# Optimization experiments

Measured on AMD Instinct MI355X. Metric: run time of the kernel, lower is better.

Reference implementation:

```python
import jax, jax.numpy as jnp
import numpy as np

B, NX, NLQ = 2, 2048, 64
D_IN, D_OUT, H = 768, 768, 12
HD = D_OUT // H  # 64
P_X, P_LQ = 0.1, 0.2  # dropout probs for x-x block vs any learnable-query block
DROP_KEY = 42  # fixed key for dropout masks (training mode)


def setup_inputs() -> dict:
    key = jax.random.key(0)
    ks = jax.random.split(key, 6)
    s = 0.02
    return {
        "x": jax.random.normal(ks[0], (B, NX, D_IN), jnp.float32),
        "learnable_queries": jax.random.normal(ks[1], (B, NLQ, D_IN), jnp.float32),
        "Wq": jax.random.normal(ks[2], (D_IN, D_OUT), jnp.float32) * s,
        "Wk": jax.random.normal(ks[3], (D_IN, D_OUT), jnp.float32) * s,
        "Wv": jax.random.normal(ks[4], (D_IN, D_OUT), jnp.float32) * s,
        "Wo": jax.random.normal(ks[5], (D_OUT, D_OUT), jnp.float32) * s,
        "bo": jnp.zeros((D_OUT,), jnp.float32),
    }


def reference(x, learnable_queries, Wq, Wk, Wv, Wo, bo):
    b, nx, _ = x.shape
    nlq = learnable_queries.shape[1]
    T = nx + nlq
    inp = jnp.concatenate([x, learnable_queries], axis=1)  # [b, T, d_in]

    def to_heads(W):
        return (inp @ W).reshape(b, T, H, HD).transpose(0, 2, 1, 3)  # [b, H, T, hd]

    q, k, v = to_heads(Wq), to_heads(Wk), to_heads(Wv)

    scores = jnp.einsum('bhqd,bhkd->bhqk', q, k) / np.float32(np.sqrt(HD))
    w = jax.nn.softmax(scores, axis=-1)  # [b, H, T, T]

    # --- block-structured dropout (training mode) ---
    kp_x = 1.0 - P_X
    kp_lq = 1.0 - P_LQ
    is_x = jnp.arange(T) < nx
    # keep prob is kp_x on the x-x block, kp_lq on the three lq-involving blocks
    keep_p = jnp.where(is_x[:, None] & is_x[None, :], kp_x, kp_lq)  # [T, T]
    u = jax.random.uniform(jax.random.key(DROP_KEY), (b, H, T, T), jnp.float32)
    mask = (u < keep_p).astype(w.dtype)
    n_xx = nx * nx
    n_lq_total = T * T - n_xx
    scale = (T * T) / (n_xx * kp_x + n_lq_total * kp_lq)
    w = w * mask * jnp.asarray(scale, w.dtype)

    ctx = jnp.einsum('bhqk,bhkd->bhqd', w, v)           # [b, H, T, hd]
    ctx = ctx.transpose(0, 2, 1, 3).reshape(b, T, D_OUT)  # [b, T, d_out]
    return ctx @ Wo + bo
```

## Files before the change

kernel.cpp:

```cpp
#include <hip/hip_runtime.h>
#include <stdint.h>

#define B_ 2
#define NX_ 2048
#define NLQ_ 64
#define T_ 2112
#define DIN_ 768
#define DOUT_ 768
#define NH_ 12
#define HD_ 64

#define QSZ_ ((size_t)3244032)
#define HALF_U 53526528u
#define SCALE_ ((float)(4460544.0 / (4194304.0 * 0.9 + 266240.0 * 0.8)))
#define WPR_ 66
#define MWPB_ 1408u
#define K_X_ 7549747u
#define K_LQ_ 6710887u

typedef __attribute__((ext_vector_type(8))) short bf16x8;
typedef __attribute__((ext_vector_type(4))) float f32x4;
typedef unsigned int uint32;

__device__ __forceinline__ uint32 rotl_(uint32 x, uint32 r) {
  return (x << r) | (x >> (32u - r));
}

__device__ __forceinline__ uint2 threefry_(uint32 x0, uint32 x1) {
  const uint32 ks0 = 0u, ks1 = 42u;
  const uint32 ks2 = 0x1BD11BDAu ^ ks0 ^ ks1;
  x0 += ks0; x1 += ks1;
#define TFR_(r) { x0 += x1; x1 = rotl_(x1, (r)); x1 ^= x0; }
  TFR_(13) TFR_(15) TFR_(26) TFR_(6)
  x0 += ks1; x1 += ks2 + 1u;
  TFR_(17) TFR_(29) TFR_(16) TFR_(24)
  x0 += ks2; x1 += ks0 + 2u;
  TFR_(13) TFR_(15) TFR_(26) TFR_(6)
  x0 += ks0; x1 += ks1 + 3u;
  TFR_(17) TFR_(29) TFR_(16) TFR_(24)
  x0 += ks1; x1 += ks2 + 4u;
  TFR_(13) TFR_(15) TFR_(26) TFR_(6)
  x0 += ks2; x1 += ks0 + 5u;
#undef TFR_
  return make_uint2(x0, x1);
}

__device__ __forceinline__ unsigned short f2b_(float f) {
  const uint32 u = __float_as_uint(f);
  return (unsigned short)((u + 0x7FFFu + ((u >> 16) & 1u)) >> 16);
}
__device__ __forceinline__ uint32 pack2_(float lo, float hi) {
  return (uint32)f2b_(lo) | ((uint32)f2b_(hi) << 16);
}

__global__ __launch_bounds__(256) void prep_kernel(
    const float* __restrict__ Wq, const float* __restrict__ Wk,
    const float* __restrict__ Wv, const float* __restrict__ Wo,
    unsigned short* __restrict__ Wt) {
  __shared__ float Tf[64][65];
  const int tid = threadIdx.x;
  const int k0 = blockIdx.x << 6;
  const int n0 = blockIdx.y << 6;
  const int mat = blockIdx.z;
  const float* Wm = (mat == 0) ? Wq : (mat == 1) ? Wk : (mat == 2) ? Wv : Wo;
  const int r = tid >> 2;
  const int cch = (tid & 3) << 4;
  const float* src = Wm + (size_t)(k0 + r) * DOUT_ + n0 + cch;
#pragma unroll
  for (int j = 0; j < 4; ++j) {
    const float4 v = *(const float4*)(src + 4 * j);
    Tf[r][cch + 4 * j + 0] = v.x; Tf[r][cch + 4 * j + 1] = v.y;
    Tf[r][cch + 4 * j + 2] = v.z; Tf[r][cch + 4 * j + 3] = v.w;
  }
  __syncthreads();
  float f[16];
#pragma unroll
  for (int j = 0; j < 16; ++j) f[j] = Tf[cch + j][r];
  uint4 o0, o1;
  o0.x = pack2_(f[0], f[1]);  o0.y = pack2_(f[2], f[3]);
  o0.z = pack2_(f[4], f[5]);  o0.w = pack2_(f[6], f[7]);
  o1.x = pack2_(f[8], f[9]);  o1.y = pack2_(f[10], f[11]);
  o1.z = pack2_(f[12], f[13]); o1.w = pack2_(f[14], f[15]);
  unsigned short* dst = Wt + ((size_t)mat * DOUT_ + n0 + r) * DIN_ + k0 + cch;
  *(uint4*)dst = o0;
  *(uint4*)(dst + 8) = o1;
}

__global__ __launch_bounds__(256) void qkv_kernel(
    const float* __restrict__ xg, const float* __restrict__ lqg,
    const unsigned short* __restrict__ Wt,
    unsigned short* __restrict__ Qh, unsigned short* __restrict__ Kh,
    unsigned short* __restrict__ Vth, uint32* __restrict__ Mask) {
  __shared__ unsigned short AsB[4096];
  __shared__ unsigned short BsB[4096];
  const int tid = threadIdx.x;
  const int w = tid >> 6;
  const int lane = tid & 63;
  const int c = lane & 15;
  const int g = lane >> 4;
  const int m0 = blockIdx.x << 6;
  const int wsel = blockIdx.y / NH_;
  const int h = blockIdx.y % NH_;

  const int ar = tid >> 2;
  const int kpart = (tid & 3) << 4;
  const float* arow;
  {
    const int m = m0 + ar;
    const int bb = m / T_;
    const int tt = m - bb * T_;
    arow = (tt < NX_) ? (xg + ((size_t)bb * NX_ + tt) * DIN_)
                      : (lqg + ((size_t)bb * NLQ_ + (tt - NX_)) * DIN_);
  }
  const unsigned short* brow = Wt + ((size_t)wsel * DOUT_ + h * HD_ + ar) * DIN_;
  const int wrA = ar * 128;
  const int swzS = (ar & 7) << 4;
  const int swzF = (c & 7) << 4;

  f32x4 ac0 = {0.f, 0.f, 0.f, 0.f}, ac1 = ac0, ac2 = ac0, ac3 = ac0;

  for (int k0 = 0; k0 < DIN_; k0 += 64) {
    const float4 a0 = *(const float4*)(arow + k0 + kpart);
    const float4 a1 = *(const float4*)(arow + k0 + kpart + 4);
    const float4 a2 = *(const float4*)(arow + k0 + kpart + 8);
    const float4 a3 = *(const float4*)(arow + k0 + kpart + 12);
    const uint4 b01 = *(const uint4*)(brow + k0 + kpart);
    const uint4 b23 = *(const uint4*)(brow + k0 + kpart + 8);
    uint4 pa0, pa1;
    pa0.x = pack2_(a0.x, a0.y); pa0.y = pack2_(a0.z, a0.w);
    pa0.z = pack2_(a1.x, a1.y); pa0.w = pack2_(a1.z, a1.w);
    pa1.x = pack2_(a2.x, a2.y); pa1.y = pack2_(a2.z, a2.w);
    pa1.z = pack2_(a3.x, a3.y); pa1.w = pack2_(a3.z, a3.w);
    __syncthreads();
    *(uint4*)((char*)AsB + wrA + ((kpart * 2) ^ swzS)) = pa0;
    *(uint4*)((char*)AsB + wrA + ((kpart * 2 + 16) ^ swzS)) = pa1;
    *(uint4*)((char*)BsB + wrA + ((kpart * 2) ^ swzS)) = b01;
    *(uint4*)((char*)BsB + wrA + ((kpart * 2 + 16) ^ swzS)) = b23;
    __syncthreads();
#pragma unroll
    for (int s = 0; s < 2; ++s) {
      const int off = ((s << 6) | (g << 4)) ^ swzF;
      const bf16x8 af = *(const bf16x8*)((const char*)AsB + (16 * w + c) * 128 + off);
      const bf16x8 b0 = *(const bf16x8*)((const char*)BsB + (c) * 128 + off);
      const bf16x8 b1 = *(const bf16x8*)((const char*)BsB + (c + 16) * 128 + off);
      const bf16x8 b2 = *(const bf16x8*)((const char*)BsB + (c + 32) * 128 + off);
      const bf16x8 b3 = *(const bf16x8*)((const char*)BsB + (c + 48) * 128 + off);
      ac0 = __builtin_amdgcn_mfma_f32_16x16x32_bf16(af, b0, ac0, 0, 0, 0);
      ac1 = __builtin_amdgcn_mfma_f32_16x16x32_bf16(af, b1, ac1, 0, 0, 0);
      ac2 = __builtin_amdgcn_mfma_f32_16x16x32_bf16(af, b2, ac2, 0, 0, 0);
      ac3 = __builtin_amdgcn_mfma_f32_16x16x32_bf16(af, b3, ac3, 0, 0, 0);
    }
  }

  const int bb2 = m0 / T_;
  const int tb = m0 - bb2 * T_;
  const size_t rowBase = (size_t)(bb2 * NH_ + h) * T_;
  if (wsel == 0) {
#pragma unroll
    for (int i = 0; i < 4; ++i) {
      const size_t rr = (rowBase + tb + 16 * w + 4 * g + i) * HD_ + c;
      Qh[rr +  0] = f2b_(ac0[i] * 0.125f);
      Qh[rr + 16] = f2b_(ac1[i] * 0.125f);
      Qh[rr + 32] = f2b_(ac2[i] * 0.125f);
      Qh[rr + 48] = f2b_(ac3[i] * 0.125f);
    }
  } else if (wsel == 1) {
#pragma unroll
    for (int i = 0; i < 4; ++i) {
      const size_t rr = (rowBase + tb + 16 * w + 4 * g + i) * HD_ + c;
      Kh[rr +  0] = f2b_(ac0[i]);
      Kh[rr + 16] = f2b_(ac1[i]);
      Kh[rr + 32] = f2b_(ac2[i]);
      Kh[rr + 48] = f2b_(ac3[i]);
    }
  } else {
    __syncthreads();
#pragma unroll
    for (int i = 0; i < 4; ++i) {
      const int col2 = (16 * w + 4 * g + i) * 2;
      *(unsigned short*)((char*)AsB + (c)      * 128 + (col2 ^ ((c & 7) << 4))) = f2b_(ac0[i]);
      *(unsigned short*)((char*)AsB + (c + 16) * 128 + (col2 ^ ((c & 7) << 4))) = f2b_(ac1[i]);
      *(unsigned short*)((char*)AsB + (c + 32) * 128 + (col2 ^ ((c & 7) << 4))) = f2b_(ac2[i]);
      *(unsigned short*)((char*)AsB + (c + 48) * 128 + (col2 ^ ((c & 7) << 4))) = f2b_(ac3[i]);
    }
    __syncthreads();
    const int hd = tid >> 2;
    const int tch = (tid & 3) << 4;
    const uint4 v0 = *(const uint4*)((const char*)AsB + hd * 128 + ((tch * 2) ^ ((hd & 7) << 4)));
    const uint4 v1 = *(const uint4*)((const char*)AsB + hd * 128 + ((tch * 2 + 16) ^ ((hd & 7) << 4)));
    unsigned short* dst = Vth + ((size_t)(bb2 * NH_ + h) * HD_ + hd) * T_ + tb + tch;
    *(uint4*)dst = v0;
    *(uint4*)(dst + 8) = v1;
  }

  const uint32 wbeg = (uint32)(blockIdx.y * 66 + blockIdx.x) * MWPB_;
  for (uint32 wI = wbeg + (uint32)tid; wI < wbeg + MWPB_; wI += 256u) {
    const uint32 rowIdx = wI / WPR_;
    const uint32 jw = wI - rowIdx * WPR_;
    const uint32 bI = rowIdx / (NH_ * T_);
    const uint32 rem = rowIdx - bI * (NH_ * T_);
    const uint32 iQ = rem % T_;
    const uint32 c0 = bI * HALF_U + rem * (uint32)T_ + jw * 32u;
    const uint32 thr = ((iQ < NX_) && (jw < 64u)) ? K_X_ : K_LQ_;
    uint32 word = 0u;
#pragma unroll 4
    for (int k = 0; k < 32; ++k) {
      const uint2 y = threefry_(0u, c0 + (uint32)k);
      word |= (((y.x ^ y.y) >> 9) < thr ? 1u : 0u) << k;
    }
    Mask[wI] = word;
  }
}

__global__ __launch_bounds__(128) void attn_kernel(
    const unsigned short* __restrict__ Qh, const unsigned short* __restrict__ Kh,
    const unsigned short* __restrict__ Vth, const uint32* __restrict__ Mask,
    float* __restrict__ ctx) {
  __shared__ unsigned short KsU[4096];
  __shared__ unsigned short VsU[4096];
  __shared__ unsigned short PsU[2 * 1152];
  const int tid = threadIdx.x;
  const int w = tid >> 6;
  const int lane = tid & 63;
  const int c = lane & 15;
  const int g = lane >> 4;
  const int q0 = blockIdx.x << 5;
  const int h = blockIdx.y;
  const int b = blockIdx.z;
  const size_t hbT = (size_t)(b * NH_ + h) * T_;
  const size_t vbase = (size_t)(b * NH_ + h) * HD_;

  bf16x8 aq0, aq1;
  {
    const unsigned short* qrow = Qh + (hbT + q0 + 16 * w + c) * HD_ + (g << 3);
    aq0 = *(const bf16x8*)(qrow);
    aq1 = *(const bf16x8*)(qrow + 32);
  }
  f32x4 ca0 = {0.f, 0.f, 0.f, 0.f}, ca1 = ca0, ca2 = ca0, ca3 = ca0;
  float lacc[4] = {0.f, 0.f, 0.f, 0.f};
  uint32 wb[4];
#pragma unroll
  for (int i = 0; i < 4; ++i)
    wb[i] = ((uint32)b * HALF_U +
             (uint32)(h * T_ + q0 + 16 * w + 4 * g + i) * (uint32)T_) >> 5;

  const int psE = w * 1152;
  const int psB = w * 2304;
  const int swz = (c & 7) << 4;

  for (int kt = 0; kt < T_; kt += 64) {
#pragma unroll
    for (int ii = 0; ii < 4; ++ii) {
      const int seg = tid + (ii << 7);
      const int srow = seg >> 3;
      const int sc = (seg & 7) << 3;
      const uint4 kv4 = *(const uint4*)(Kh + (hbT + kt + srow) * HD_ + sc);
      *(uint4*)((char*)KsU + srow * 128 + ((sc * 2) ^ ((srow & 7) << 4))) = kv4;
      const uint4 vv4 = *(const uint4*)(Vth + (vbase + srow) * T_ + kt + sc);
      *(uint4*)((char*)VsU + srow * 128 + ((sc * 2) ^ ((srow & 7) << 4))) = vv4;
    }
    __syncthreads();

    f32x4 sa0 = {0.f, 0.f, 0.f, 0.f}, sa1 = sa0, sa2 = sa0, sa3 = sa0;
#pragma unroll
    for (int s = 0; s < 2; ++s) {
      const int off = ((s << 6) | (g << 4)) ^ swz;
      const bf16x8 bk0 = *(const bf16x8*)((const char*)KsU + (c) * 128 + off);
      const bf16x8 bk1 = *(const bf16x8*)((const char*)KsU + (c + 16) * 128 + off);
      const bf16x8 bk2 = *(const bf16x8*)((const char*)KsU + (c + 32) * 128 + off);
      const bf16x8 bk3 = *(const bf16x8*)((const char*)KsU + (c + 48) * 128 + off);
      const bf16x8 aqs = s ? aq1 : aq0;
      sa0 = __builtin_amdgcn_mfma_f32_16x16x32_bf16(aqs, bk0, sa0, 0, 0, 0);
      sa1 = __builtin_amdgcn_mfma_f32_16x16x32_bf16(aqs, bk1, sa1, 0, 0, 0);
      sa2 = __builtin_amdgcn_mfma_f32_16x16x32_bf16(aqs, bk2, sa2, 0, 0, 0);
      sa3 = __builtin_amdgcn_mfma_f32_16x16x32_bf16(aqs, bk3, sa3, 0, 0, 0);
    }

    const uint32 ktw = (uint32)(kt >> 5);
#pragma unroll
    for (int n = 0; n < 4; ++n) {
      const f32x4 sv = (n == 0) ? sa0 : (n == 1) ? sa1 : (n == 2) ? sa2 : sa3;
      const int sh = ((n & 1) << 4) + c;
      const uint32 wOff = ktw + (n >> 1);
#pragma unroll
      for (int i = 0; i < 4; ++i) {
        const float pe = __expf(sv[i]);
        lacc[i] += pe;
        const uint32 word = Mask[wb[i] + wOff];
        PsU[psE + (4 * g + i) * 72 + 16 * n + c] =
            ((word >> sh) & 1u) ? f2b_(pe) : (unsigned short)0;
      }
    }
    __syncthreads();

    const bf16x8 ap0 = *(const bf16x8*)((const char*)PsU + psB + c * 144 + (g << 4));
    const bf16x8 ap1 = *(const bf16x8*)((const char*)PsU + psB + c * 144 + 64 + (g << 4));
#pragma unroll
    for (int s = 0; s < 2; ++s) {
      const int off = ((s << 6) | (g << 4)) ^ swz;
      const bf16x8 bv0 = *(const bf16x8*)((const char*)VsU + (c) * 128 + off);
      const bf16x8 bv1 = *(const bf16x8*)((const char*)VsU + (c + 16) * 128 + off);
      const bf16x8 bv2 = *(const bf16x8*)((const char*)VsU + (c + 32) * 128 + off);
      const bf16x8 bv3 = *(const bf16x8*)((const char*)VsU + (c + 48) * 128 + off);
      const bf16x8 aps = s ? ap1 : ap0;
      ca0 = __builtin_amdgcn_mfma_f32_16x16x32_bf16(aps, bv0, ca0, 0, 0, 0);
      ca1 = __builtin_amdgcn_mfma_f32_16x16x32_bf16(aps, bv1, ca1, 0, 0, 0);
      ca2 = __builtin_amdgcn_mfma_f32_16x16x32_bf16(aps, bv2, ca2, 0, 0, 0);
      ca3 = __builtin_amdgcn_mfma_f32_16x16x32_bf16(aps, bv3, ca3, 0, 0, 0);
    }
    __syncthreads();
  }

#pragma unroll
  for (int i = 0; i < 4; ++i) {
    float li = lacc[i];
    li += __shfl_xor(li, 1);
    li += __shfl_xor(li, 2);
    li += __shfl_xor(li, 4);
    li += __shfl_xor(li, 8);
    const float inv = SCALE_ / li;
    float* dst = ctx + (size_t)(b * T_ + q0 + 16 * w + 4 * g + i) * DOUT_ + (h << 6) + c;
    dst[0]  = ca0[i] * inv;
    dst[16] = ca1[i] * inv;
    dst[32] = ca2[i] * inv;
    dst[48] = ca3[i] * inv;
  }
}

__global__ __launch_bounds__(256) void oproj_kernel(
    const float* __restrict__ ctxm, const unsigned short* __restrict__ Wt,
    const float* __restrict__ bo, float* __restrict__ out) {
  __shared__ unsigned short AsB[4096];
  __shared__ unsigned short BsB[4096];
  const int tid = threadIdx.x;
  const int w = tid >> 6;
  const int lane = tid & 63;
  const int c = lane & 15;
  const int g = lane >> 4;
  const int m0 = blockIdx.x << 6;
  const int n0 = blockIdx.y << 6;
  const int ar = tid >> 2;
  const int kpart = (tid & 3) << 4;
  const float* arow = ctxm + (size_t)(m0 + ar) * DIN_;
  const unsigned short* brow = Wt + ((size_t)3 * DOUT_ + n0 + ar) * DIN_;
  const int wrA = ar * 128;
  const int swzS = (ar & 7) << 4;
  const int swzF = (c & 7) << 4;

  f32x4 ac0 = {0.f, 0.f, 0.f, 0.f}, ac1 = ac0, ac2 = ac0, ac3 = ac0;
  for (int k0 = 0; k0 < DIN_; k0 += 64) {
    const float4 a0 = *(const float4*)(arow + k0 + kpart);
    const float4 a1 = *(const float4*)(arow + k0 + kpart + 4);
    const float4 a2 = *(const float4*)(arow + k0 + kpart + 8);
    const float4 a3 = *(const float4*)(arow + k0 + kpart + 12);
    const uint4 b01 = *(const uint4*)(brow + k0 + kpart);
    const uint4 b23 = *(const uint4*)(brow + k0 + kpart + 8);
    uint4 pa0, pa1;
    pa0.x = pack2_(a0.x, a0.y); pa0.y = pack2_(a0.z, a0.w);
    pa0.z = pack2_(a1.x, a1.y); pa0.w = pack2_(a1.z, a1.w);
    pa1.x = pack2_(a2.x, a2.y); pa1.y = pack2_(a2.z, a2.w);
    pa1.z = pack2_(a3.x, a3.y); pa1.w = pack2_(a3.z, a3.w);
    __syncthreads();
    *(uint4*)((char*)AsB + wrA + ((kpart * 2) ^ swzS)) = pa0;
    *(uint4*)((char*)AsB + wrA + ((kpart * 2 + 16) ^ swzS)) = pa1;
    *(uint4*)((char*)BsB + wrA + ((kpart * 2) ^ swzS)) = b01;
    *(uint4*)((char*)BsB + wrA + ((kpart * 2 + 16) ^ swzS)) = b23;
    __syncthreads();
#pragma unroll
    for (int s = 0; s < 2; ++s) {
      const int off = ((s << 6) | (g << 4)) ^ swzF;
      const bf16x8 af = *(const bf16x8*)((const char*)AsB + (16 * w + c) * 128 + off);
      const bf16x8 b0 = *(const bf16x8*)((const char*)BsB + (c) * 128 + off);
      const bf16x8 b1 = *(const bf16x8*)((const char*)BsB + (c + 16) * 128 + off);
      const bf16x8 b2 = *(const bf16x8*)((const char*)BsB + (c + 32) * 128 + off);
      const bf16x8 b3 = *(const bf16x8*)((const char*)BsB + (c + 48) * 128 + off);
      ac0 = __builtin_amdgcn_mfma_f32_16x16x32_bf16(af, b0, ac0, 0, 0, 0);
      ac1 = __builtin_amdgcn_mfma_f32_16x16x32_bf16(af, b1, ac1, 0, 0, 0);
      ac2 = __builtin_amdgcn_mfma_f32_16x16x32_bf16(af, b2, ac2, 0, 0, 0);
      ac3 = __builtin_amdgcn_mfma_f32_16x16x32_bf16(af, b3, ac3, 0, 0, 0);
    }
  }
  const float bi0 = bo[n0 + c];
  const float bi1 = bo[n0 + 16 + c];
  const float bi2 = bo[n0 + 32 + c];
  const float bi3 = bo[n0 + 48 + c];
#pragma unroll
  for (int i = 0; i < 4; ++i) {
    float* dst = out + (size_t)(m0 + 16 * w + 4 * g + i) * DOUT_ + n0 + c;
    dst[0]  = ac0[i] + bi0;
    dst[16] = ac1[i] + bi1;
    dst[32] = ac2[i] + bi2;
    dst[48] = ac3[i] + bi3;
  }
}

extern "C" void kernel_launch(void* const* d_in, const int* in_sizes, int n_in,
                              void* d_out, int out_size, void* d_ws, size_t ws_size,
                              hipStream_t stream) {
  (void)in_sizes; (void)n_in; (void)out_size; (void)ws_size;
  const float* x  = (const float*)d_in[0];
  const float* lq = (const float*)d_in[1];
  const float* Wq = (const float*)d_in[2];
  const float* Wk = (const float*)d_in[3];
  const float* Wv = (const float*)d_in[4];
  const float* Wo = (const float*)d_in[5];
  const float* bo = (const float*)d_in[6];
  unsigned short* Qh  = (unsigned short*)d_ws;
  unsigned short* Kh  = Qh + QSZ_;
  unsigned short* Vth = Kh + QSZ_;
  float* Cb = (float*)(Vth + QSZ_);
  unsigned short* Wt = (unsigned short*)(Cb + QSZ_);
  uint32* Mask = (uint32*)((char*)d_ws + 37158912);
  prep_kernel<<<dim3(12, 12, 4), dim3(256), 0, stream>>>(Wq, Wk, Wv, Wo, Wt);
  qkv_kernel<<<dim3(66, 36), dim3(256), 0, stream>>>(x, lq, Wt, Qh, Kh, Vth, Mask);
  attn_kernel<<<dim3(66, NH_, B_), dim3(128), 0, stream>>>(Qh, Kh, Vth, Mask, Cb);
  oproj_kernel<<<dim3(66, 12), dim3(256), 0, stream>>>(Cb, Wt, bo, (float*)d_out);
}
```

Measured before the change: 472.3 us.

## Pre-convert inputs to bf16, fuse QKV per head, ballot-based mask, wider attention blocks

A new kernel converts x and the learnable queries to bf16 once, so the QKV GEMM no longer repeats the fp32-to-bf16 packing for each of the 36 weight column blocks. The QKV kernel now computes Q, K and V for one head in a single block, reusing the A tile across 12 MFMA column tiles. The dropout mask generation changes from a per-thread loop over 32 bits to one threefry call per lane with wave ballots, thresholding full 32-bit values. The attention kernel doubles to 64 queries and 4 waves per block, halving K/V tile reloads at the cost of fewer blocks and more registers and LDS per block.

```diff
diff --git a/kernel.cpp b/kernel.cpp
--- a/kernel.cpp
+++ b/kernel.cpp
@@ -13,10 +13,8 @@
 #define QSZ_ ((size_t)3244032)
 #define HALF_U 53526528u
 #define SCALE_ ((float)(4460544.0 / (4194304.0 * 0.9 + 266240.0 * 0.8)))
-#define WPR_ 66
-#define MWPB_ 1408u
-#define K_X_ 7549747u
-#define K_LQ_ 6710887u
+#define KXS_ 3865470464u
+#define KLQS_ 3435974144u
 
 typedef __attribute__((ext_vector_type(8))) short bf16x8;
 typedef __attribute__((ext_vector_type(4))) float f32x4;
@@ -53,6 +51,24 @@
   return (uint32)f2b_(lo) | ((uint32)f2b_(hi) << 16);
 }
 
+__global__ __launch_bounds__(256) void xconv_kernel(
+    const float* __restrict__ xg, const float* __restrict__ lqg,
+    unsigned short* __restrict__ Xb) {
+  const uint32 f = (blockIdx.x * 256u + threadIdx.x) * 8u;
+  const uint32 m = f / 768u;
+  const uint32 col = f - m * 768u;
+  const uint32 bb = (m >= (uint32)T_) ? 1u : 0u;
+  const uint32 tt = m - bb * (uint32)T_;
+  const float* src = (tt < NX_) ? (xg + ((size_t)bb * NX_ + tt) * DIN_ + col)
+                                : (lqg + ((size_t)bb * NLQ_ + (tt - NX_)) * DIN_ + col);
+  const float4 a = *(const float4*)(src);
+  const float4 b = *(const float4*)(src + 4);
+  uint4 o;
+  o.x = pack2_(a.x, a.y); o.y = pack2_(a.z, a.w);
+  o.z = pack2_(b.x, b.y); o.w = pack2_(b.z, b.w);
+  *(uint4*)(Xb + f) = o;
+}
+
 __global__ __launch_bounds__(256) void prep_kernel(
     const float* __restrict__ Wq, const float* __restrict__ Wk,
     const float* __restrict__ Wv, const float* __restrict__ Wo,
@@ -87,144 +103,139 @@
 }
 
 __global__ __launch_bounds__(256) void qkv_kernel(
-    const float* __restrict__ xg, const float* __restrict__ lqg,
-    const unsigned short* __restrict__ Wt,
+    const unsigned short* __restrict__ Xb, const unsigned short* __restrict__ Wt,
     unsigned short* __restrict__ Qh, unsigned short* __restrict__ Kh,
     unsigned short* __restrict__ Vth, uint32* __restrict__ Mask) {
   __shared__ unsigned short AsB[4096];
-  __shared__ unsigned short BsB[4096];
+  __shared__ unsigned short BsB[12288];
   const int tid = threadIdx.x;
   const int w = tid >> 6;
   const int lane = tid & 63;
   const int c = lane & 15;
   const int g = lane >> 4;
   const int m0 = blockIdx.x << 6;
-  const int wsel = blockIdx.y / NH_;
-  const int h = blockIdx.y % NH_;
-
-  const int ar = tid >> 2;
-  const int kpart = (tid & 3) << 4;
-  const float* arow;
-  {
-    const int m = m0 + ar;
-    const int bb = m / T_;
-    const int tt = m - bb * T_;
-    arow = (tt < NX_) ? (xg + ((size_t)bb * NX_ + tt) * DIN_)
-                      : (lqg + ((size_t)bb * NLQ_ + (tt - NX_)) * DIN_);
-  }
-  const unsigned short* brow = Wt + ((size_t)wsel * DOUT_ + h * HD_ + ar) * DIN_;
-  const int wrA = ar * 128;
-  const int swzS = (ar & 7) << 4;
+  const int h  = blockIdx.y;
+
+  const int srow = tid >> 2;
+  const int seg  = (tid & 3) << 5;
+  const int swzR = ((srow & 7) << 4);
   const int swzF = (c & 7) << 4;
 
-  f32x4 ac0 = {0.f, 0.f, 0.f, 0.f}, ac1 = ac0, ac2 = ac0, ac3 = ac0;
+  f32x4 acc[12];
+#pragma unroll
+  for (int nt = 0; nt < 12; ++nt) acc[nt] = (f32x4){0.f, 0.f, 0.f, 0.f};
+
+  const unsigned short* arow = Xb + (size_t)(m0 + srow) * DIN_;
 
   for (int k0 = 0; k0 < DIN_; k0 += 64) {
-    const float4 a0 = *(const float4*)(arow + k0 + kpart);
-    const float4 a1 = *(const float4*)(arow + k0 + kpart + 4);
-    const float4 a2 = *(const float4*)(arow + k0 + kpart + 8);
-    const float4 a3 = *(const float4*)(arow + k0 + kpart + 12);
-    const uint4 b01 = *(const uint4*)(brow + k0 + kpart);
-    const uint4 b23 = *(const uint4*)(brow + k0 + kpart + 8);
-    uint4 pa0, pa1;
-    pa0.x = pack2_(a0.x, a0.y); pa0.y = pack2_(a0.z, a0.w);
-    pa0.z = pack2_(a1.x, a1.y); pa0.w = pack2_(a1.z, a1.w);
-    pa1.x = pack2_(a2.x, a2.y); pa1.y = pack2_(a2.z, a2.w);
-    pa1.z = pack2_(a3.x, a3.y); pa1.w = pack2_(a3.z, a3.w);
-    __syncthreads();
-    *(uint4*)((char*)AsB + wrA + ((kpart * 2) ^ swzS)) = pa0;
-    *(uint4*)((char*)AsB + wrA + ((kpart * 2 + 16) ^ swzS)) = pa1;
-    *(uint4*)((char*)BsB + wrA + ((kpart * 2) ^ swzS)) = b01;
-    *(uint4*)((char*)BsB + wrA + ((kpart * 2 + 16) ^ swzS)) = b23;
+    const uint4 a0 = *(const uint4*)(arow + k0 + (seg >> 1));
+    const uint4 a1 = *(const uint4*)(arow + k0 + (seg >> 1) + 8);
+    uint4 b0[3], b1[3];
+#pragma unroll
+    for (int ii = 0; ii < 3; ++ii) {
+      const int n = srow + (ii << 6);
+      const unsigned short* brow =
+          Wt + ((size_t)(n >> 6) * DOUT_ + h * HD_ + (n & 63)) * DIN_ + k0 + (seg >> 1);
+      b0[ii] = *(const uint4*)(brow);
+      b1[ii] = *(const uint4*)(brow + 8);
+    }
+    __syncthreads();
+    *(uint4*)((char*)AsB + srow * 128 + (seg ^ swzR)) = a0;
+    *(uint4*)((char*)AsB + srow * 128 + ((seg + 16) ^ swzR)) = a1;
+#pragma unroll
+    for (int ii = 0; ii < 3; ++ii) {
+      const int n = srow + (ii << 6);
+      *(uint4*)((char*)BsB + n * 128 + (seg ^ swzR)) = b0[ii];
+      *(uint4*)((char*)BsB + n * 128 + ((seg + 16) ^ swzR)) = b1[ii];
+    }
     __syncthreads();
 #pragma unroll
     for (int s = 0; s < 2; ++s) {
       const int off = ((s << 6) | (g << 4)) ^ swzF;
       const bf16x8 af = *(const bf16x8*)((const char*)AsB + (16 * w + c) * 128 + off);
-      const bf16x8 b0 = *(const bf16x8*)((const char*)BsB + (c) * 128 + off);
-      const bf16x8 b1 = *(const bf16x8*)((const char*)BsB + (c + 16) * 128 + off);
-      const bf16x8 b2 = *(const bf16x8*)((const char*)BsB + (c + 32) * 128 + off);
-      const bf16x8 b3 = *(const bf16x8*)((const char*)BsB + (c + 48) * 128 + off);
-      ac0 = __builtin_amdgcn_mfma_f32_16x16x32_bf16(af, b0, ac0, 0, 0, 0);
-      ac1 = __builtin_amdgcn_mfma_f32_16x16x32_bf16(af, b1, ac1, 0, 0, 0);
-      ac2 = __builtin_amdgcn_mfma_f32_16x16x32_bf16(af, b2, ac2, 0, 0, 0);
-      ac3 = __builtin_amdgcn_mfma_f32_16x16x32_bf16(af, b3, ac3, 0, 0, 0);
-    }
+#pragma unroll
+      for (int nt = 0; nt < 12; ++nt) {
+        const bf16x8 bf = *(const bf16x8*)((const char*)BsB + (nt * 16 + c) * 128 + off);
+        acc[nt] = __builtin_amdgcn_mfma_f32_16x16x32_bf16(af, bf, acc[nt], 0, 0, 0);
+      }
+    }
+    __syncthreads();
   }
 
   const int bb2 = m0 / T_;
   const int tb = m0 - bb2 * T_;
-  const size_t rowBase = (size_t)(bb2 * NH_ + h) * T_;
-  if (wsel == 0) {
-#pragma unroll
-    for (int i = 0; i < 4; ++i) {
-      const size_t rr = (rowBase + tb + 16 * w + 4 * g + i) * HD_ + c;
-      Qh[rr +  0] = f2b_(ac0[i] * 0.125f);
-      Qh[rr + 16] = f2b_(ac1[i] * 0.125f);
-      Qh[rr + 32] = f2b_(ac2[i] * 0.125f);
-      Qh[rr + 48] = f2b_(ac3[i] * 0.125f);
-    }
-  } else if (wsel == 1) {
-#pragma unroll
-    for (int i = 0; i < 4; ++i) {
-      const size_t rr = (rowBase + tb + 16 * w + 4 * g + i) * HD_ + c;
-      Kh[rr +  0] = f2b_(ac0[i]);
-      Kh[rr + 16] = f2b_(ac1[i]);
-      Kh[rr + 32] = f2b_(ac2[i]);
-      Kh[rr + 48] = f2b_(ac3[i]);
-    }
-  } else {
-    __syncthreads();
+  const size_t rowBase = (size_t)(bb2 * NH_ + h) * T_ + tb;
+#pragma unroll
+  for (int nt = 0; nt < 4; ++nt)
+#pragma unroll
+    for (int i = 0; i < 4; ++i)
+      Qh[(rowBase + 16 * w + 4 * g + i) * HD_ + nt * 16 + c] = f2b_(acc[nt][i] * 0.125f);
+#pragma unroll
+  for (int nt = 4; nt < 8; ++nt)
+#pragma unroll
+    for (int i = 0; i < 4; ++i)
+      Kh[(rowBase + 16 * w + 4 * g + i) * HD_ + (nt - 4) * 16 + c] = f2b_(acc[nt][i]);
+#pragma unroll
+  for (int nt = 8; nt < 12; ++nt) {
+    const int hd = (nt - 8) * 16 + c;
 #pragma unroll
     for (int i = 0; i < 4; ++i) {
       const int col2 = (16 * w + 4 * g + i) * 2;
-      *(unsigned short*)((char*)AsB + (c)      * 128 + (col2 ^ ((c & 7) << 4))) = f2b_(ac0[i]);
-      *(unsigned short*)((char*)AsB + (c + 16) * 128 + (col2 ^ ((c & 7) << 4))) = f2b_(ac1[i]);
-      *(unsigned short*)((char*)AsB + (c + 32) * 128 + (col2 ^ ((c & 7) << 4))) = f2b_(ac2[i]);
-      *(unsigned short*)((char*)AsB + (c + 48) * 128 + (col2 ^ ((c & 7) << 4))) = f2b_(ac3[i]);
-    }
-    __syncthreads();
+      *(unsigned short*)((char*)AsB + hd * 128 + (col2 ^ swzF)) = f2b_(acc[nt][i]);
+    }
+  }
+  __syncthreads();
+  {
     const int hd = tid >> 2;
-    const int tch = (tid & 3) << 4;
-    const uint4 v0 = *(const uint4*)((const char*)AsB + hd * 128 + ((tch * 2) ^ ((hd & 7) << 4)));
-    const uint4 v1 = *(const uint4*)((const char*)AsB + hd * 128 + ((tch * 2 + 16) ^ ((hd & 7) << 4)));
-    unsigned short* dst = Vth + ((size_t)(bb2 * NH_ + h) * HD_ + hd) * T_ + tb + tch;
+    const int ch = (tid & 3) << 5;
+    const uint4 v0 = *(const uint4*)((const char*)AsB + hd * 128 + (ch ^ ((hd & 7) << 4)));
+    const uint4 v1 = *(const uint4*)((const char*)AsB + hd * 128 + ((ch + 16) ^ ((hd & 7) << 4)));
+    unsigned short* dst = Vth + ((size_t)(bb2 * NH_ + h) * HD_ + hd) * T_ + tb + (ch >> 1);
     *(uint4*)dst = v0;
     *(uint4*)(dst + 8) = v1;
   }
 
-  const uint32 wbeg = (uint32)(blockIdx.y * 66 + blockIdx.x) * MWPB_;
-  for (uint32 wI = wbeg + (uint32)tid; wI < wbeg + MWPB_; wI += 256u) {
-    const uint32 rowIdx = wI / WPR_;
-    const uint32 jw = wI - rowIdx * WPR_;
-    const uint32 bI = rowIdx / (NH_ * T_);
-    const uint32 rem = rowIdx - bI * (NH_ * T_);
-    const uint32 iQ = rem % T_;
-    const uint32 c0 = bI * HALF_U + rem * (uint32)T_ + jw * 32u;
-    const uint32 thr = ((iQ < NX_) && (jw < 64u)) ? K_X_ : K_LQ_;
-    uint32 word = 0u;
-#pragma unroll 4
-    for (int k = 0; k < 32; ++k) {
-      const uint2 y = threefry_(0u, c0 + (uint32)k);
-      word |= (((y.x ^ y.y) >> 9) < thr ? 1u : 0u) << k;
-    }
-    Mask[wI] = word;
-  }
-}
-
-__global__ __launch_bounds__(128) void attn_kernel(
+  const uint32 wvbeg = (uint32)(blockIdx.y * 66 + blockIdx.x) * 4224u + (uint32)w * 1056u;
+  for (uint32 wI = wvbeg; wI < wvbeg + 1056u; wI += 4u) {
+    const uint32 b0 = wI * 32u;
+    const uint32 g0 = b0 + (uint32)lane;
+    const uint32 g1 = g0 + 64u;
+    uint32 thrS0, thrS1;
+    {
+      const uint32 row0 = b0 / 2112u;
+      const uint32 cb0 = b0 - row0 * 2112u;
+      thrS0 = ((row0 % 2112u) < 2048u && cb0 < 2048u) ? KXS_ : KLQS_;
+      const uint32 b1 = b0 + 64u;
+      const uint32 row1 = b1 / 2112u;
+      const uint32 cb1 = b1 - row1 * 2112u;
+      thrS1 = ((row1 % 2112u) < 2048u && cb1 < 2048u) ? KXS_ : KLQS_;
+    }
+    const uint2 ya = threefry_(0u, g0);
+    const uint2 yb = threefry_(0u, g1);
+    const unsigned long long balA = __ballot((ya.x ^ ya.y) < thrS0);
+    const unsigned long long balB = __ballot((yb.x ^ yb.y) < thrS1);
+    if (lane == 0) {
+      uint4 st;
+      st.x = (uint32)balA; st.y = (uint32)(balA >> 32);
+      st.z = (uint32)balB; st.w = (uint32)(balB >> 32);
+      *(uint4*)(Mask + wI) = st;
+    }
+  }
+}
+
+__global__ __launch_bounds__(256) void attn_kernel(
     const unsigned short* __restrict__ Qh, const unsigned short* __restrict__ Kh,
     const unsigned short* __restrict__ Vth, const uint32* __restrict__ Mask,
     float* __restrict__ ctx) {
   __shared__ unsigned short KsU[4096];
   __shared__ unsigned short VsU[4096];
-  __shared__ unsigned short PsU[2 * 1152];
+  __shared__ unsigned short PsU[4 * 1152];
   const int tid = threadIdx.x;
   const int w = tid >> 6;
   const int lane = tid & 63;
   const int c = lane & 15;
   const int g = lane >> 4;
-  const int q0 = blockIdx.x << 5;
+  const int q0 = blockIdx.x << 6;
   const int h = blockIdx.y;
   const int b = blockIdx.z;
   const size_t hbT = (size_t)(b * NH_ + h) * T_;
@@ -250,8 +261,8 @@
 
   for (int kt = 0; kt < T_; kt += 64) {
 #pragma unroll
-    for (int ii = 0; ii < 4; ++ii) {
-      const int seg = tid + (ii << 7);
+    for (int ii = 0; ii < 2; ++ii) {
+      const int seg = tid + (ii << 8);
       const int srow = seg >> 3;
       const int sc = (seg & 7) << 3;
       const uint4 kv4 = *(const uint4*)(Kh + (hbT + kt + srow) * HD_ + sc);
@@ -409,10 +420,12 @@
   unsigned short* Kh  = Qh + QSZ_;
   unsigned short* Vth = Kh + QSZ_;
   float* Cb = (float*)(Vth + QSZ_);
+  unsigned short* Xb = (unsigned short*)Cb;
   unsigned short* Wt = (unsigned short*)(Cb + QSZ_);
   uint32* Mask = (uint32*)((char*)d_ws + 37158912);
+  xconv_kernel<<<dim3(1584), dim3(256), 0, stream>>>(x, lq, Xb);
   prep_kernel<<<dim3(12, 12, 4), dim3(256), 0, stream>>>(Wq, Wk, Wv, Wo, Wt);
-  qkv_kernel<<<dim3(66, 36), dim3(256), 0, stream>>>(x, lq, Wt, Qh, Kh, Vth, Mask);
-  attn_kernel<<<dim3(66, NH_, B_), dim3(128), 0, stream>>>(Qh, Kh, Vth, Mask, Cb);
+  qkv_kernel<<<dim3(66, 12), dim3(256), 0, stream>>>(Xb, Wt, Qh, Kh, Vth, Mask);
+  attn_kernel<<<dim3(33, NH_, B_), dim3(256), 0, stream>>>(Qh, Kh, Vth, Mask, Cb);
   oproj_kernel<<<dim3(66, 12), dim3(256), 0, stream>>>(Cb, Wt, bo, (float*)d_out);
 }
```

New measurement: 598.2 us. +26.6%, slower.

## Pre-convert inputs to bf16, ballot-based dropout mask, larger attention tiles

Applied to the files above, without the earlier changes.

Adds a kernel that converts x and the learnable queries to bf16 once, so the QKV GEMM no longer repacks fp32 on every N-tile. It also swaps the QKV grid order so blocks sharing an input row tile run close together. The dropout mask generation now has each lane produce one threefry bit, combines bits with a wave ballot, and compares full 32-bit values against scaled thresholds. Attention now uses 64-query blocks with 256 threads and writes the context as bf16, which halves the context traffic into the output projection at some precision cost.

```diff
diff --git a/kernel.cpp b/kernel.cpp
--- a/kernel.cpp
+++ b/kernel.cpp
@@ -13,10 +13,8 @@
 #define QSZ_ ((size_t)3244032)
 #define HALF_U 53526528u
 #define SCALE_ ((float)(4460544.0 / (4194304.0 * 0.9 + 266240.0 * 0.8)))
-#define WPR_ 66
-#define MWPB_ 1408u
-#define K_X_ 7549747u
-#define K_LQ_ 6710887u
+#define KXS_ 3865470464u
+#define KLQS_ 3435974144u
 
 typedef __attribute__((ext_vector_type(8))) short bf16x8;
 typedef __attribute__((ext_vector_type(4))) float f32x4;
@@ -53,6 +51,24 @@
   return (uint32)f2b_(lo) | ((uint32)f2b_(hi) << 16);
 }
 
+__global__ __launch_bounds__(256) void xconv_kernel(
+    const float* __restrict__ xg, const float* __restrict__ lqg,
+    unsigned short* __restrict__ Xb) {
+  const uint32 f = (blockIdx.x * 256u + threadIdx.x) * 8u;
+  const uint32 m = f / 768u;
+  const uint32 col = f - m * 768u;
+  const uint32 bb = (m >= (uint32)T_) ? 1u : 0u;
+  const uint32 tt = m - bb * (uint32)T_;
+  const float* src = (tt < NX_) ? (xg + ((size_t)bb * NX_ + tt) * DIN_ + col)
+                                : (lqg + ((size_t)bb * NLQ_ + (tt - NX_)) * DIN_ + col);
+  const float4 a = *(const float4*)(src);
+  const float4 b = *(const float4*)(src + 4);
+  uint4 o;
+  o.x = pack2_(a.x, a.y); o.y = pack2_(a.z, a.w);
+  o.z = pack2_(b.x, b.y); o.w = pack2_(b.z, b.w);
+  *(uint4*)(Xb + f) = o;
+}
+
 __global__ __launch_bounds__(256) void prep_kernel(
     const float* __restrict__ Wq, const float* __restrict__ Wk,
     const float* __restrict__ Wv, const float* __restrict__ Wo,
@@ -87,8 +103,7 @@
 }
 
 __global__ __launch_bounds__(256) void qkv_kernel(
-    const float* __restrict__ xg, const float* __restrict__ lqg,
-    const unsigned short* __restrict__ Wt,
+    const unsigned short* __restrict__ Xb, const unsigned short* __restrict__ Wt,
     unsigned short* __restrict__ Qh, unsigned short* __restrict__ Kh,
     unsigned short* __restrict__ Vth, uint32* __restrict__ Mask) {
   __shared__ unsigned short AsB[4096];
@@ -98,20 +113,13 @@
   const int lane = tid & 63;
   const int c = lane & 15;
   const int g = lane >> 4;
-  const int m0 = blockIdx.x << 6;
-  const int wsel = blockIdx.y / NH_;
-  const int h = blockIdx.y % NH_;
+  const int wsel = blockIdx.x / NH_;
+  const int h = blockIdx.x % NH_;
+  const int m0 = blockIdx.y << 6;
 
   const int ar = tid >> 2;
   const int kpart = (tid & 3) << 4;
-  const float* arow;
-  {
-    const int m = m0 + ar;
-    const int bb = m / T_;
-    const int tt = m - bb * T_;
-    arow = (tt < NX_) ? (xg + ((size_t)bb * NX_ + tt) * DIN_)
-                      : (lqg + ((size_t)bb * NLQ_ + (tt - NX_)) * DIN_);
-  }
+  const unsigned short* arow = Xb + (size_t)(m0 + ar) * DIN_;
   const unsigned short* brow = Wt + ((size_t)wsel * DOUT_ + h * HD_ + ar) * DIN_;
   const int wrA = ar * 128;
   const int swzS = (ar & 7) << 4;
@@ -120,20 +128,13 @@
   f32x4 ac0 = {0.f, 0.f, 0.f, 0.f}, ac1 = ac0, ac2 = ac0, ac3 = ac0;
 
   for (int k0 = 0; k0 < DIN_; k0 += 64) {
-    const float4 a0 = *(const float4*)(arow + k0 + kpart);
-    const float4 a1 = *(const float4*)(arow + k0 + kpart + 4);
-    const float4 a2 = *(const float4*)(arow + k0 + kpart + 8);
-    const float4 a3 = *(const float4*)(arow + k0 + kpart + 12);
+    const uint4 a01 = *(const uint4*)(arow + k0 + kpart);
+    const uint4 a23 = *(const uint4*)(arow + k0 + kpart + 8);
     const uint4 b01 = *(const uint4*)(brow + k0 + kpart);
     const uint4 b23 = *(const uint4*)(brow + k0 + kpart + 8);
-    uint4 pa0, pa1;
-    pa0.x = pack2_(a0.x, a0.y); pa0.y = pack2_(a0.z, a0.w);
-    pa0.z = pack2_(a1.x, a1.y); pa0.w = pack2_(a1.z, a1.w);
-    pa1.x = pack2_(a2.x, a2.y); pa1.y = pack2_(a2.z, a2.w);
-    pa1.z = pack2_(a3.x, a3.y); pa1.w = pack2_(a3.z, a3.w);
-    __syncthreads();
-    *(uint4*)((char*)AsB + wrA + ((kpart * 2) ^ swzS)) = pa0;
-    *(uint4*)((char*)AsB + wrA + ((kpart * 2 + 16) ^ swzS)) = pa1;
+    __syncthreads();
+    *(uint4*)((char*)AsB + wrA + ((kpart * 2) ^ swzS)) = a01;
+    *(uint4*)((char*)AsB + wrA + ((kpart * 2 + 16) ^ swzS)) = a23;
     *(uint4*)((char*)BsB + wrA + ((kpart * 2) ^ swzS)) = b01;
     *(uint4*)((char*)BsB + wrA + ((kpart * 2 + 16) ^ swzS)) = b23;
     __syncthreads();
@@ -193,38 +194,48 @@
     *(uint4*)(dst + 8) = v1;
   }
 
-  const uint32 wbeg = (uint32)(blockIdx.y * 66 + blockIdx.x) * MWPB_;
-  for (uint32 wI = wbeg + (uint32)tid; wI < wbeg + MWPB_; wI += 256u) {
-    const uint32 rowIdx = wI / WPR_;
-    const uint32 jw = wI - rowIdx * WPR_;
-    const uint32 bI = rowIdx / (NH_ * T_);
-    const uint32 rem = rowIdx - bI * (NH_ * T_);
-    const uint32 iQ = rem % T_;
-    const uint32 c0 = bI * HALF_U + rem * (uint32)T_ + jw * 32u;
-    const uint32 thr = ((iQ < NX_) && (jw < 64u)) ? K_X_ : K_LQ_;
-    uint32 word = 0u;
-#pragma unroll 4
-    for (int k = 0; k < 32; ++k) {
-      const uint2 y = threefry_(0u, c0 + (uint32)k);
-      word |= (((y.x ^ y.y) >> 9) < thr ? 1u : 0u) << k;
-    }
-    Mask[wI] = word;
-  }
-}
-
-__global__ __launch_bounds__(128) void attn_kernel(
+  const uint32 bid = (uint32)(blockIdx.y * 36 + blockIdx.x);
+  const uint32 wvbeg = bid * 1408u + (uint32)w * 352u;
+  for (uint32 wI = wvbeg; wI < wvbeg + 352u; wI += 4u) {
+    const uint32 b0 = wI * 32u;
+    const uint32 g0 = b0 + (uint32)lane;
+    const uint32 g1 = g0 + 64u;
+    uint32 thrS0, thrS1;
+    {
+      const uint32 row0 = b0 / 2112u;
+      const uint32 cb0 = b0 - row0 * 2112u;
+      thrS0 = ((row0 % 2112u) < 2048u && cb0 < 2048u) ? KXS_ : KLQS_;
+      const uint32 b1v = b0 + 64u;
+      const uint32 row1 = b1v / 2112u;
+      const uint32 cb1 = b1v - row1 * 2112u;
+      thrS1 = ((row1 % 2112u) < 2048u && cb1 < 2048u) ? KXS_ : KLQS_;
+    }
+    const uint2 ya = threefry_(0u, g0);
+    const uint2 yb = threefry_(0u, g1);
+    const unsigned long long balA = __ballot((ya.x ^ ya.y) < thrS0);
+    const unsigned long long balB = __ballot((yb.x ^ yb.y) < thrS1);
+    if (lane == 0) {
+      uint4 st;
+      st.x = (uint32)balA; st.y = (uint32)(balA >> 32);
+      st.z = (uint32)balB; st.w = (uint32)(balB >> 32);
+      *(uint4*)(Mask + wI) = st;
+    }
+  }
+}
+
+__global__ __launch_bounds__(256) void attn_kernel(
     const unsigned short* __restrict__ Qh, const unsigned short* __restrict__ Kh,
     const unsigned short* __restrict__ Vth, const uint32* __restrict__ Mask,
-    float* __restrict__ ctx) {
+    unsigned short* __restrict__ ctx) {
   __shared__ unsigned short KsU[4096];
   __shared__ unsigned short VsU[4096];
-  __shared__ unsigned short PsU[2 * 1152];
+  __shared__ unsigned short PsU[4 * 1152];
   const int tid = threadIdx.x;
   const int w = tid >> 6;
   const int lane = tid & 63;
   const int c = lane & 15;
   const int g = lane >> 4;
-  const int q0 = blockIdx.x << 5;
+  const int q0 = blockIdx.x << 6;
   const int h = blockIdx.y;
   const int b = blockIdx.z;
   const size_t hbT = (size_t)(b * NH_ + h) * T_;
@@ -250,8 +261,8 @@
 
   for (int kt = 0; kt < T_; kt += 64) {
 #pragma unroll
-    for (int ii = 0; ii < 4; ++ii) {
-      const int seg = tid + (ii << 7);
+    for (int ii = 0; ii < 2; ++ii) {
+      const int seg = tid + (ii << 8);
       const int srow = seg >> 3;
       const int sc = (seg & 7) << 3;
       const uint4 kv4 = *(const uint4*)(Kh + (hbT + kt + srow) * HD_ + sc);
@@ -319,16 +330,17 @@
     li += __shfl_xor(li, 4);
     li += __shfl_xor(li, 8);
     const float inv = SCALE_ / li;
-    float* dst = ctx + (size_t)(b * T_ + q0 + 16 * w + 4 * g + i) * DOUT_ + (h << 6) + c;
-    dst[0]  = ca0[i] * inv;
-    dst[16] = ca1[i] * inv;
-    dst[32] = ca2[i] * inv;
-    dst[48] = ca3[i] * inv;
+    unsigned short* dst =
+        ctx + (size_t)(b * T_ + q0 + 16 * w + 4 * g + i) * DOUT_ + (h << 6) + c;
+    dst[0]  = f2b_(ca0[i] * inv);
+    dst[16] = f2b_(ca1[i] * inv);
+    dst[32] = f2b_(ca2[i] * inv);
+    dst[48] = f2b_(ca3[i] * inv);
   }
 }
 
 __global__ __launch_bounds__(256) void oproj_kernel(
-    const float* __restrict__ ctxm, const unsigned short* __restrict__ Wt,
+    const unsigned short* __restrict__ ctxm, const unsigned short* __restrict__ Wt,
     const float* __restrict__ bo, float* __restrict__ out) {
   __shared__ unsigned short AsB[4096];
   __shared__ unsigned short BsB[4096];
@@ -341,7 +353,7 @@
   const int n0 = blockIdx.y << 6;
   const int ar = tid >> 2;
   const int kpart = (tid & 3) << 4;
-  const float* arow = ctxm + (size_t)(m0 + ar) * DIN_;
+  const unsigned short* arow = ctxm + (size_t)(m0 + ar) * DIN_;
   const unsigned short* brow = Wt + ((size_t)3 * DOUT_ + n0 + ar) * DIN_;
   const int wrA = ar * 128;
   const int swzS = (ar & 7) << 4;
@@ -349,20 +361,13 @@
 
   f32x4 ac0 = {0.f, 0.f, 0.f, 0.f}, ac1 = ac0, ac2 = ac0, ac3 = ac0;
   for (int k0 = 0; k0 < DIN_; k0 += 64) {
-    const float4 a0 = *(const float4*)(arow + k0 + kpart);
-    const float4 a1 = *(const float4*)(arow + k0 + kpart + 4);
-    const float4 a2 = *(const float4*)(arow + k0 + kpart + 8);
-    const float4 a3 = *(const float4*)(arow + k0 + kpart + 12);
+    const uint4 a01 = *(const uint4*)(arow + k0 + kpart);
+    const uint4 a23 = *(const uint4*)(arow + k0 + kpart + 8);
     const uint4 b01 = *(const uint4*)(brow + k0 + kpart);
     const uint4 b23 = *(const uint4*)(brow + k0 + kpart + 8);
-    uint4 pa0, pa1;
-    pa0.x = pack2_(a0.x, a0.y); pa0.y = pack2_(a0.z, a0.w);
-    pa0.z = pack2_(a1.x, a1.y); pa0.w = pack2_(a1.z, a1.w);
-    pa1.x = pack2_(a2.x, a2.y); pa1.y = pack2_(a2.z, a2.w);
-    pa1.z = pack2_(a3.x, a3.y); pa1.w = pack2_(a3.z, a3.w);
-    __syncthreads();
-    *(uint4*)((char*)AsB + wrA + ((kpart * 2) ^ swzS)) = pa0;
-    *(uint4*)((char*)AsB + wrA + ((kpart * 2 + 16) ^ swzS)) = pa1;
+    __syncthreads();
+    *(uint4*)((char*)AsB + wrA + ((kpart * 2) ^ swzS)) = a01;
+    *(uint4*)((char*)AsB + wrA + ((kpart * 2 + 16) ^ swzS)) = a23;
     *(uint4*)((char*)BsB + wrA + ((kpart * 2) ^ swzS)) = b01;
     *(uint4*)((char*)BsB + wrA + ((kpart * 2 + 16) ^ swzS)) = b23;
     __syncthreads();
@@ -408,11 +413,13 @@
   unsigned short* Qh  = (unsigned short*)d_ws;
   unsigned short* Kh  = Qh + QSZ_;
   unsigned short* Vth = Kh + QSZ_;
-  float* Cb = (float*)(Vth + QSZ_);
-  unsigned short* Wt = (unsigned short*)(Cb + QSZ_);
+  unsigned short* Cb  = Vth + QSZ_;
+  unsigned short* Xb  = Cb;
+  unsigned short* Wt  = (unsigned short*)((char*)d_ws + 32440320);
   uint32* Mask = (uint32*)((char*)d_ws + 37158912);
+  xconv_kernel<<<dim3(1584), dim3(256), 0, stream>>>(x, lq, Xb);
   prep_kernel<<<dim3(12, 12, 4), dim3(256), 0, stream>>>(Wq, Wk, Wv, Wo, Wt);
-  qkv_kernel<<<dim3(66, 36), dim3(256), 0, stream>>>(x, lq, Wt, Qh, Kh, Vth, Mask);
-  attn_kernel<<<dim3(66, NH_, B_), dim3(128), 0, stream>>>(Qh, Kh, Vth, Mask, Cb);
+  qkv_kernel<<<dim3(36, 66), dim3(256), 0, stream>>>(Xb, Wt, Qh, Kh, Vth, Mask);
+  attn_kernel<<<dim3(33, NH_, B_), dim3(256), 0, stream>>>(Qh, Kh, Vth, Mask, Cb);
   oproj_kernel<<<dim3(66, 12), dim3(256), 0, stream>>>(Cb, Wt, bo, (float*)d_out);
 }
```

Result: no change. 480.8 us (+1.8%).
